# Optimization experiments

Measured on AMD Instinct MI355X. Metric: run time of the kernel, lower is better.

The kernel has to match this reference:

```python
import jax, jax.numpy as jnp
import numpy as np

B, N, C = 32, 197, 768   # batch, tokens (num_patches+1), emb_dim
KW = 197                 # kw_dim = seq_len
L = 12                   # num_layers (weights shared, norms per-layer)
HID = 3072               # mlp hidden = 4*emb_dim


def layer_norm(x, g, b, eps=1e-5):
    mu = jnp.mean(x, axis=-1, keepdims=True)
    var = jnp.var(x, axis=-1, keepdims=True)
    return (x - mu) * jax.lax.rsqrt(var + eps) * g + b


def attention(x, qkv_w, fc_w, fc_b, ln_g, ln_b, fc2_w, fc2_b, num_heads):
    b, n, c = x.shape
    d = c // num_heads
    qkv = (x @ qkv_w).reshape(b, n, 3, num_heads, d)
    q = qkv[:, :, 0].transpose(0, 2, 1, 3)  # [B,H,N,d]
    k = qkv[:, :, 1].transpose(0, 2, 1, 3)
    v = qkv[:, :, 2].transpose(0, 2, 1, 3)
    scale = d ** -0.5
    attn = jnp.einsum('bhnd,bhmd->bhnm', q, k) * scale      # [B,H,N,N]
    attn = attn @ fc_w + fc_b                                # [B,H,N,KW]
    attn = layer_norm(attn, ln_g, ln_b)
    attn = jax.nn.softmax(attn, axis=-1)
    attn = attn.transpose(0, 1, 3, 2)                        # [B,H,KW,N]
    y = jnp.einsum('bhkn,bhnd->bhkd', attn, v)               # [B,H,KW,d]
    # fc2 applied along KW axis of y.transpose(-2,-1): out[b,h,n,d]
    out = jnp.einsum('bhkd,kn->bnhd', y, fc2_w) + fc2_b[None, :, None, None]
    return out.reshape(b, n, c)


def mlp(x, w1, b1, w2, b2):
    return jax.nn.gelu(x @ w1 + b1, approximate=False) @ w2 + b2


def setup_inputs() -> dict:
    key = jax.random.key(0)
    ks = jax.random.split(key, 16)
    s = 0.02
    return {
        'x': jax.random.normal(ks[0], (B, N, C), jnp.float32),
        'qkv_w': jax.random.normal(ks[1], (C, 3 * C), jnp.float32) * s,
        'fc_w': jax.random.normal(ks[2], (N, KW), jnp.float32) * s,
        'fc_b': jnp.zeros((KW,), jnp.float32),
        'attn_ln_g': jnp.ones((KW,), jnp.float32),
        'attn_ln_b': jnp.zeros((KW,), jnp.float32),
        'fc2_w': jax.random.normal(ks[3], (KW, N), jnp.float32) * s,
        'fc2_b': jnp.zeros((N,), jnp.float32),
        'mlp_w1': jax.random.normal(ks[4], (C, HID), jnp.float32) * s,
        'mlp_b1': jnp.zeros((HID,), jnp.float32),
        'mlp_w2': jax.random.normal(ks[5], (HID, C), jnp.float32) * s,
        'mlp_b2': jnp.zeros((C,), jnp.float32),
        'f_ln_g': jnp.ones((L, C), jnp.float32),
        'f_ln_b': jnp.zeros((L, C), jnp.float32),
        'g_ln_g': jnp.ones((L, C), jnp.float32),
        'g_ln_b': jnp.zeros((L, C), jnp.float32),
        'num_heads': 12,
    }


def reference(x, qkv_w, fc_w, fc_b, attn_ln_g, attn_ln_b, fc2_w, fc2_b,
              mlp_w1, mlp_b1, mlp_w2, mlp_b2, f_ln_g, f_ln_b, g_ln_g, g_ln_b,
              num_heads):
    # x -> cat([x,x]) -> reversible stack -> mean of the two halves
    x1, x2 = x, x
    n_layers = f_ln_g.shape[0]
    for i in range(n_layers):
        # y1 = x1 + f(x2); y2 = x2 + g(y1)  (PreNorm wraps f and g)
        y1 = x1 + attention(layer_norm(x2, f_ln_g[i], f_ln_b[i]),
                            qkv_w, fc_w, fc_b, attn_ln_g, attn_ln_b,
                            fc2_w, fc2_b, num_heads)
        y2 = x2 + mlp(layer_norm(y1, g_ln_g[i], g_ln_b[i]),
                      mlp_w1, mlp_b1, mlp_w2, mlp_b2)
        x1, x2 = y1, y2
    return (x1 + x2) * 0.5
```

## Files before the change

### kernel.cpp

```cpp
#include <hip/hip_runtime.h>
#include <math.h>

#define BB   32
#define NN   197
#define CC   768
#define HH   12
#define DD   64
#define KWW  197
#define HIDD 3072
#define NL   12
#define RR   (BB*NN)
#define BHH  (BB*HH)
#define NP   224
#define SLS  232

typedef __attribute__((ext_vector_type(8))) short short8;
typedef __attribute__((ext_vector_type(4))) float floatx4;
typedef __attribute__((ext_vector_type(4))) unsigned short us4;

__device__ __forceinline__ unsigned short f2bf(float f) {
    unsigned int u = __float_as_uint(f);
    u += 0x7fff + ((u >> 16) & 1);
    return (unsigned short)(u >> 16);
}

__global__ void ln768_kernel(const float* __restrict__ in, const float* __restrict__ g,
                             const float* __restrict__ be, unsigned short* __restrict__ out) {
    int row = blockIdx.x;
    int t = threadIdx.x;
    float4 v = ((const float4*)(in + (size_t)row * CC))[t];
    float s = v.x+v.y+v.z+v.w;
    float q = v.x*v.x+v.y*v.y+v.z*v.z+v.w*v.w;
    for (int off = 1; off < 64; off <<= 1) {
        s += __shfl_xor(s, off, 64);
        q += __shfl_xor(q, off, 64);
    }
    __shared__ float sh[6];
    int wv = t >> 6, ln = t & 63;
    if (ln == 0) { sh[wv] = s; sh[3+wv] = q; }
    __syncthreads();
    s = sh[0]+sh[1]+sh[2];
    q = sh[3]+sh[4]+sh[5];
    float mu  = s * (1.0f/CC);
    float var = q * (1.0f/CC) - mu*mu;
    float rs  = rsqrtf(var + 1e-5f);
    float4 gv = ((const float4*)g)[t];
    float4 bv = ((const float4*)be)[t];
    us4 o = { f2bf((v.x-mu)*rs*gv.x + bv.x), f2bf((v.y-mu)*rs*gv.y + bv.y),
              f2bf((v.z-mu)*rs*gv.z + bv.z), f2bf((v.w-mu)*rs*gv.w + bv.w) };
    *(us4*)(out + (size_t)row*CC + t*4) = o;
}

__global__ void init_ln(const float* __restrict__ x, float* __restrict__ x1,
                        float* __restrict__ x2,
                        const float* __restrict__ g, const float* __restrict__ be,
                        unsigned short* __restrict__ out) {
    int row = blockIdx.x;
    int t = threadIdx.x;
    float4 v = ((const float4*)(x + (size_t)row * CC))[t];
    ((float4*)(x1 + (size_t)row * CC))[t] = v;
    ((float4*)(x2 + (size_t)row * CC))[t] = v;
    float s = v.x+v.y+v.z+v.w;
    float q = v.x*v.x+v.y*v.y+v.z*v.z+v.w*v.w;
    for (int off = 1; off < 64; off <<= 1) {
        s += __shfl_xor(s, off, 64);
        q += __shfl_xor(q, off, 64);
    }
    __shared__ float sh[6];
    int wv = t >> 6, ln = t & 63;
    if (ln == 0) { sh[wv] = s; sh[3+wv] = q; }
    __syncthreads();
    s = sh[0]+sh[1]+sh[2];
    q = sh[3]+sh[4]+sh[5];
    float mu  = s * (1.0f/CC);
    float var = q * (1.0f/CC) - mu*mu;
    float rs  = rsqrtf(var + 1e-5f);
    float4 gv = ((const float4*)g)[t];
    float4 bv = ((const float4*)be)[t];
    us4 o = { f2bf((v.x-mu)*rs*gv.x + bv.x), f2bf((v.y-mu)*rs*gv.y + bv.y),
              f2bf((v.z-mu)*rs*gv.z + bv.z), f2bf((v.w-mu)*rs*gv.w + bv.w) };
    *(us4*)(out + (size_t)row*CC + t*4) = o;
}

__global__ void reduce_ln(float* __restrict__ x2, const float* __restrict__ part,
                          const float* __restrict__ b2,
                          const float* __restrict__ g, const float* __restrict__ be,
                          unsigned short* __restrict__ out,
                          const float* __restrict__ x1f, float* __restrict__ outf,
                          int mode) {
    int row = blockIdx.x;
    int t = threadIdx.x;
    float4 v  = ((float4*)(x2 + (size_t)row * CC))[t];
    float4 a0 = ((const float4*)(part + (size_t)row * CC))[t];
    float4 a1 = ((const float4*)(part + (size_t)RR*CC + (size_t)row * CC))[t];
    float4 bb = ((const float4*)b2)[t];
    v.x += a0.x + a1.x + bb.x;
    v.y += a0.y + a1.y + bb.y;
    v.z += a0.z + a1.z + bb.z;
    v.w += a0.w + a1.w + bb.w;
    ((float4*)(x2 + (size_t)row * CC))[t] = v;
    if (mode == 2) {
        float4 xo = ((const float4*)(x1f + (size_t)row * CC))[t];
        float4 o;
        o.x = 0.5f*(xo.x + v.x); o.y = 0.5f*(xo.y + v.y);
        o.z = 0.5f*(xo.z + v.z); o.w = 0.5f*(xo.w + v.w);
        ((float4*)(outf + (size_t)row * CC))[t] = o;
        return;
    }
    float s = v.x+v.y+v.z+v.w;
    float q = v.x*v.x+v.y*v.y+v.z*v.z+v.w*v.w;
    for (int off = 1; off < 64; off <<= 1) {
        s += __shfl_xor(s, off, 64);
        q += __shfl_xor(q, off, 64);
    }
    __shared__ float sh[6];
    int wv = t >> 6, ln = t & 63;
    if (ln == 0) { sh[wv] = s; sh[3+wv] = q; }
    __syncthreads();
    s = sh[0]+sh[1]+sh[2];
    q = sh[3]+sh[4]+sh[5];
    float mu  = s * (1.0f/CC);
    float var = q * (1.0f/CC) - mu*mu;
    float rs  = rsqrtf(var + 1e-5f);
    float4 gv = ((const float4*)g)[t];
    float4 bv = ((const float4*)be)[t];
    us4 o = { f2bf((v.x-mu)*rs*gv.x + bv.x), f2bf((v.y-mu)*rs*gv.y + bv.y),
              f2bf((v.z-mu)*rs*gv.z + bv.z), f2bf((v.w-mu)*rs*gv.w + bv.w) };
    *(us4*)(out + (size_t)row*CC + t*4) = o;
}

__global__ void transpose_cast(const float* __restrict__ in, unsigned short* __restrict__ out,
                               int K, int Nd, int Kpad) {
    __shared__ float tile[32][33];
    int n0 = blockIdx.x*32, k0 = blockIdx.y*32;
    int tx = threadIdx.x & 31, ty = threadIdx.x >> 5;
    #pragma unroll
    for (int i = 0; i < 4; i++) {
        int k = k0 + ty + i*8;
        tile[ty + i*8][tx] = (k < K && n0+tx < Nd) ? in[(size_t)k*Nd + n0 + tx] : 0.f;
    }
    __syncthreads();
    #pragma unroll
    for (int i = 0; i < 4; i++) {
        int n = n0 + ty + i*8;
        if (n < Nd && k0 + tx < Kpad) out[(size_t)n*Kpad + k0 + tx] = f2bf(tile[tx][ty + i*8]);
    }
}

template<int EPI, int KS>
__global__ __launch_bounds__(256) void gemm128(
    const unsigned short* __restrict__ A, const unsigned short* __restrict__ Bt,
    const float* __restrict__ bias, float* __restrict__ Cf, unsigned short* __restrict__ Cb,
    int M, int Nd, int K)
{
    __shared__ unsigned short As[128*64];
    __shared__ unsigned short Bs[128*64];
    int tid  = threadIdx.x;
    int wv   = tid >> 6, lane = tid & 63;
    int wm   = wv >> 1, wn = wv & 1;
    int quad = lane >> 4, mrow = lane & 15;
    int rl   = lane >> 3, ps = lane & 7;

    int gx   = gridDim.x;
    int nwg  = gx * gridDim.y;
    int orig = blockIdx.y * gx + blockIdx.x;
    int qq = nwg >> 3, rr = nwg & 7;
    int xcd = orig & 7, idx = orig >> 3;
    int wg  = (xcd < rr ? xcd*(qq+1) : rr*(qq+1) + (xcd-rr)*qq) + idx;
    int bm  = (wg / gx) * 128;
    int bn  = (wg % gx) * 128;

    const int Kc    = K / KS;
    const int kbase = (KS > 1) ? blockIdx.z * Kc : 0;

    floatx4 acc[4][4];
    #pragma unroll
    for (int i = 0; i < 4; i++)
        #pragma unroll
        for (int j = 0; j < 4; j++) acc[i][j] = (floatx4){0.f,0.f,0.f,0.f};

    for (int k0 = kbase; k0 < kbase + Kc; k0 += 64) {
        #pragma unroll
        for (int i = 0; i < 4; i++) {
            int r_ = wv*32 + i*8 + rl;
            int sl = ps ^ (r_ & 7);
            int gr = bm + r_; if (gr > M-1) gr = M-1;
            __builtin_amdgcn_global_load_lds(
                (const __attribute__((address_space(1))) void*)(A + (size_t)gr*K + k0 + sl*8),
                (__attribute__((address_space(3))) void*)(As + (wv*32 + i*8)*64),
                16, 0, 0);
        }
        #pragma unroll
        for (int i = 0; i < 4; i++) {
            int r_ = wv*32 + i*8 + rl;
            int sl = ps ^ (r_ & 7);
            int gr = bn + r_;
            __builtin_amdgcn_global_load_lds(
                (const __attribute__((address_space(1))) void*)(Bt + (size_t)gr*K + k0 + sl*8),
                (__attribute__((address_space(3))) void*)(Bs + (wv*32 + i*8)*64),
                16, 0, 0);
        }
        __syncthreads();
        #pragma unroll
        for (int kk = 0; kk < 2; kk++) {
            short8 af[4], bf[4];
            #pragma unroll
            for (int mi = 0; mi < 4; mi++) {
                int lr = wm*64 + mi*16 + mrow;
                af[mi] = *(const short8*)&As[lr*64 + (((kk<<2)|quad) ^ (lr & 7))*8];
            }
            #pragma unroll
            for (int ni = 0; ni < 4; ni++) {
                int lr = wn*64 + ni*16 + mrow;
                bf[ni] = *(const short8*)&Bs[lr*64 + (((kk<<2)|quad) ^ (lr & 7))*8];
            }
            #pragma unroll
            for (int mi = 0; mi < 4; mi++)
                #pragma unroll
                for (int ni = 0; ni < 4; ni++)
                    acc[mi][ni] = __builtin_amdgcn_mfma_f32_16x16x32_bf16(
                        af[mi], bf[ni], acc[mi][ni], 0, 0, 0);
        }
        __syncthreads();
    }

    float* Cfz = (EPI == 5) ? (Cf + (size_t)blockIdx.z * M * Nd) : Cf;
    #pragma unroll
    for (int mi = 0; mi < 4; mi++) {
        int row0 = bm + wm*64 + mi*16 + quad*4;
        int bA[4], nA[4];
        if (EPI == 4) {
            int b0 = row0 / NN, n0 = row0 - b0*NN;
            #pragma unroll
            for (int r = 0; r < 4; r++) {
                bA[r] = b0; nA[r] = n0;
                n0++; if (n0 == NN) { n0 = 0; b0++; }
            }
        }
        #pragma unroll
        for (int ni = 0; ni < 4; ni++) {
            int col = bn + wn*64 + ni*16 + mrow;
            float bv = (EPI == 2) ? bias[col] : 0.f;
            #pragma unroll
            for (int r = 0; r < 4; r++) {
                int row = row0 + r;
                if (row >= M) continue;
                float v = acc[mi][ni][r] + bv;
                if (EPI == 2) {
                    v = v / (1.0f + __expf(-1.5957691216f*v*(1.0f + 0.044715f*v*v)));
                    Cb[(size_t)row*Nd + col] = f2bf(v);
                } else if (EPI == 5) {
                    Cfz[(size_t)row*Nd + col] = v;
                } else if (EPI == 4) {
                    int sel = col / CC;
                    int rem = col - sel*CC;
                    int h = rem >> 6, d = rem & 63;
                    int bh = bA[r]*HH + h;
                    unsigned short val = f2bf(v);
                    if (sel < 2)
                        Cb[((size_t)sel*BHH + bh)*NN*DD + (size_t)nA[r]*DD + d] = val;
                    else
                        Cb[(size_t)2*BHH*NN*DD + (size_t)bh*DD*NP + (size_t)d*NP + nA[r]] = val;
                }
            }
        }
    }
}

__global__ __launch_bounds__(256) void attn_score(
    const unsigned short* __restrict__ qb,
    const unsigned short* __restrict__ kb,
    const unsigned short* __restrict__ fw,
    const float* __restrict__ fbias,
    const float* __restrict__ g, const float* __restrict__ be,
    unsigned short* __restrict__ PT)
{
    int bh = blockIdx.y;
    int bm = blockIdx.x * 64;
    __shared__ unsigned short Ks[224*DD];
    __shared__ unsigned short S1s[64*SLS];
    __shared__ unsigned short Bs[224*32];
    __shared__ float gls[NP], bls[NP], bbs[NP];
    int tid = threadIdx.x;
    if (tid < NP) {
        bool vc = tid < KWW;
        gls[tid] = vc ? g[tid]     : 1.f;
        bls[tid] = vc ? be[tid]    : 0.f;
        bbs[tid] = vc ? fbias[tid] : 0.f;
    }
    int wv = tid >> 6, lane = tid & 63;
    int quad = lane >> 4, mrow = lane & 15;

    {
        int lrow = lane >> 3, lsl = lane & 7;
        #pragma unroll
        for (int i = 0; i < 7; i++) {
            int r = wv*56 + i*8 + lrow;
            int lko = (lsl ^ (r & 7)) * 8;
            __builtin_amdgcn_global_load_lds(
                (const __attribute__((address_space(1))) void*)(kb + ((size_t)bh*NN + r)*DD + lko),
                (__attribute__((address_space(3))) void*)(Ks + (size_t)(wv*56 + i*8)*DD),
                16, 0, 0);
        }
    }
    int qrow = bm + wv*16 + mrow; if (qrow > NN-1) qrow = NN-1;
    short8 aq0 = *(const short8*)&qb[((size_t)bh*NN + qrow)*DD + quad*8];
    short8 aq1 = *(const short8*)&qb[((size_t)bh*NN + qrow)*DD + 32 + quad*8];
    __syncthreads();

    #pragma unroll
    for (int ni = 0; ni < 14; ni++) {
        floatx4 a = (floatx4){0.f,0.f,0.f,0.f};
        int lr = ni*16 + mrow;
        short8 bf0 = *(const short8*)&Ks[(size_t)lr*DD + ((quad    ) ^ (lr & 7))*8];
        short8 bf1 = *(const short8*)&Ks[(size_t)lr*DD + ((4 + quad) ^ (lr & 7))*8];
        a = __builtin_amdgcn_mfma_f32_16x16x32_bf16(aq0, bf0, a, 0, 0, 0);
        a = __builtin_amdgcn_mfma_f32_16x16x32_bf16(aq1, bf1, a, 0, 0, 0);
        #pragma unroll
        for (int r = 0; r < 4; r++)
            S1s[(size_t)(wv*16 + quad*4 + r)*SLS + ni*16 + mrow] = f2bf(a[r]*0.125f);
    }
    __syncthreads();

    floatx4 acc[14];
    #pragma unroll
    for (int j = 0; j < 14; j++) acc[j] = (floatx4){0.f,0.f,0.f,0.f};
    for (int k0 = 0; k0 < 7; k0++) {
        for (int c = wv; c < 14; c += 4) {
            int r_ = c*16 + (lane >> 2);
            int gr = r_; if (gr > KWW-1) gr = KWW-1;
            int sl = ((lane & 3) ^ (r_ & 3)) * 8;
            __builtin_amdgcn_global_load_lds(
                (const __attribute__((address_space(1))) void*)(fw + (size_t)gr*NP + k0*32 + sl),
                (__attribute__((address_space(3))) void*)(Bs + (size_t)(c*16)*32),
                16, 0, 0);
        }
        __syncthreads();
        short8 af = *(const short8*)&S1s[(size_t)(wv*16 + mrow)*SLS + k0*32 + quad*8];
        #pragma unroll
        for (int ni = 0; ni < 14; ni++) {
            int lr = ni*16 + mrow;
            short8 bf = *(const short8*)&Bs[(size_t)lr*32 + (quad ^ (lr & 3))*8];
            acc[ni] = __builtin_amdgcn_mfma_f32_16x16x32_bf16(af, bf, acc[ni], 0, 0, 0);
        }
        __syncthreads();
    }

    float s[4] = {}, q[4] = {};
    #pragma unroll
    for (int ni = 0; ni < 14; ni++) {
        int col = ni*16 + mrow;
        float cm = (col < KWW) ? 1.f : 0.f;
        #pragma unroll
        for (int r = 0; r < 4; r++) {
            float x = acc[ni][r] + bbs[col];
            acc[ni][r] = x;
            s[r] += x*cm; q[r] += x*x*cm;
        }
    }
    #pragma unroll
    for (int o = 1; o < 16; o <<= 1)
        #pragma unroll
        for (int r = 0; r < 4; r++) {
            s[r] += __shfl_xor(s[r], o, 64);
            q[r] += __shfl_xor(q[r], o, 64);
        }
    float mu[4], rs[4], mx[4];
    #pragma unroll
    for (int r = 0; r < 4; r++) {
        mu[r] = s[r] * (1.0f/KWW);
        float var = q[r] * (1.0f/KWW) - mu[r]*mu[r];
        rs[r] = rsqrtf(var + 1e-5f);
        mx[r] = -1e30f;
    }
    #pragma unroll
    for (int ni = 0; ni < 14; ni++) {
        int col = ni*16 + mrow;
        bool vc = col < KWW;
        #pragma unroll
        for (int r = 0; r < 4; r++) {
            float x = (acc[ni][r] - mu[r]) * rs[r] * gls[col] + bls[col];
            acc[ni][r] = x;
            if (vc) mx[r] = fmaxf(mx[r], x);
        }
    }
    #pragma unroll
    for (int o = 1; o < 16; o <<= 1)
        #pragma unroll
        for (int r = 0; r < 4; r++)
            mx[r] = fmaxf(mx[r], __shfl_xor(mx[r], o, 64));
    float se[4] = {};
    #pragma unroll
    for (int ni = 0; ni < 14; ni++) {
        int col = ni*16 + mrow;
        float cm = (col < KWW) ? 1.f : 0.f;
        #pragma unroll
        for (int r = 0; r < 4; r++) {
            float p = __expf(acc[ni][r] - mx[r]) * cm;
            acc[ni][r] = p;
            se[r] += p;
        }
    }
    #pragma unroll
    for (int o = 1; o < 16; o <<= 1)
        #pragma unroll
        for (int r = 0; r < 4; r++)
            se[r] += __shfl_xor(se[r], o, 64);
    unsigned short* Pb = PT + (size_t)bh*NP*NP;
    int row0 = bm + wv*16 + quad*4;
    float inv0 = 1.0f/se[0], inv1 = 1.0f/se[1], inv2 = 1.0f/se[2], inv3 = 1.0f/se[3];
    #pragma unroll
    for (int ni = 0; ni < 14; ni++) {
        int col = ni*16 + mrow;
        if (col >= KWW) continue;
        if (row0 + 3 < NN) {
            us4 o = { f2bf(acc[ni][0]*inv0), f2bf(acc[ni][1]*inv1),
                      f2bf(acc[ni][2]*inv2), f2bf(acc[ni][3]*inv3) };
            *(us4*)&Pb[(size_t)col*NP + row0] = o;
        } else {
            float invs[4] = {inv0, inv1, inv2, inv3};
            #pragma unroll
            for (int r = 0; r < 4; r++)
                if (row0 + r < NN)
                    Pb[(size_t)col*NP + row0 + r] = f2bf(acc[ni][r]*invs[r]);
        }
    }
}

__global__ __launch_bounds__(256) void attn_out2(
    const unsigned short* __restrict__ PT,
    const unsigned short* __restrict__ vT,
    const unsigned short* __restrict__ fw,
    const float* __restrict__ bias,
    float* __restrict__ x1)
{
    int dt = blockIdx.x;
    int bh = blockIdx.y; int b = bh / HH, h = bh - b*HH;
    __shared__ unsigned short yT[16*232];
    int wv = threadIdx.x >> 6, lane = threadIdx.x & 63;
    int quad = lane >> 4, mrow = lane & 15;
    const unsigned short* Pb = PT + (size_t)bh*NP*NP;
    const unsigned short* Vb = vT + (size_t)bh*DD*NP + (size_t)(dt*16)*NP;

    short8 bfv[7];
    #pragma unroll
    for (int kc = 0; kc < 7; kc++)
        bfv[kc] = *(const short8*)&Vb[(size_t)mrow*NP + kc*32 + quad*8];
    #pragma unroll
    for (int i = 0; i < 2; i++) {
        int t0 = wv + i*8, t1 = t0 + 4;
        bool v1 = t1 < 14;
        floatx4 a0 = (floatx4){0.f,0.f,0.f,0.f};
        floatx4 a1 = (floatx4){0.f,0.f,0.f,0.f};
        #pragma unroll
        for (int kc = 0; kc < 7; kc++) {
            short8 p0 = *(const short8*)&Pb[(size_t)(t0*16 + mrow)*NP + kc*32 + quad*8];
            a0 = __builtin_amdgcn_mfma_f32_16x16x32_bf16(p0, bfv[kc], a0, 0, 0, 0);
            if (v1) {
                short8 p1 = *(const short8*)&Pb[(size_t)(t1*16 + mrow)*NP + kc*32 + quad*8];
                a1 = __builtin_amdgcn_mfma_f32_16x16x32_bf16(p1, bfv[kc], a1, 0, 0, 0);
            }
        }
        us4 o0 = { f2bf(a0[0]), f2bf(a0[1]), f2bf(a0[2]), f2bf(a0[3]) };
        *(us4*)&yT[mrow*232 + t0*16 + quad*4] = o0;
        if (v1) {
            us4 o1 = { f2bf(a1[0]), f2bf(a1[1]), f2bf(a1[2]), f2bf(a1[3]) };
            *(us4*)&yT[mrow*232 + t1*16 + quad*4] = o1;
        }
    }
    __syncthreads();

    short8 yf[7];
    #pragma unroll
    for (int kc = 0; kc < 7; kc++)
        yf[kc] = *(const short8*)&yT[mrow*232 + kc*32 + quad*8];
    float* xb = x1 + (size_t)b*NN*CC + (size_t)h*DD + dt*16 + mrow;
    #pragma unroll
    for (int i = 0; i < 2; i++) {
        int n0t = wv + i*8, n1t = n0t + 4;
        bool v1 = n1t < 13;
        floatx4 a0 = (floatx4){0.f,0.f,0.f,0.f};
        floatx4 a1 = (floatx4){0.f,0.f,0.f,0.f};
        #pragma unroll
        for (int kc = 0; kc < 7; kc++) {
            short8 f0 = *(const short8*)&fw[(size_t)(n0t*16 + mrow)*NP + kc*32 + quad*8];
            a0 = __builtin_amdgcn_mfma_f32_16x16x32_bf16(f0, yf[kc], a0, 0, 0, 0);
            if (v1) {
                short8 f1 = *(const short8*)&fw[(size_t)(n1t*16 + mrow)*NP + kc*32 + quad*8];
                a1 = __builtin_amdgcn_mfma_f32_16x16x32_bf16(f1, yf[kc], a1, 0, 0, 0);
            }
        }
        #pragma unroll
        for (int r = 0; r < 4; r++) {
            int n = n0t*16 + quad*4 + r;
            if (n < NN) xb[(size_t)n*CC] += a0[r] + bias[n];
        }
        if (v1) {
            #pragma unroll
            for (int r = 0; r < 4; r++) {
                int n = n1t*16 + quad*4 + r;
                if (n < NN) xb[(size_t)n*CC] += a1[r] + bias[n];
            }
        }
    }
}

extern "C" void kernel_launch(void* const* d_in, const int* in_sizes, int n_in,
                              void* d_out, int out_size, void* d_ws, size_t ws_size,
                              hipStream_t stream) {
    const float* x     = (const float*)d_in[0];
    const float* qkv_w = (const float*)d_in[1];
    const float* fc_w  = (const float*)d_in[2];
    const float* fc_b  = (const float*)d_in[3];
    const float* alng  = (const float*)d_in[4];
    const float* alnb  = (const float*)d_in[5];
    const float* fc2w  = (const float*)d_in[6];
    const float* fc2b  = (const float*)d_in[7];
    const float* w1    = (const float*)d_in[8];
    const float* b1    = (const float*)d_in[9];
    const float* w2    = (const float*)d_in[10];
    const float* b2    = (const float*)d_in[11];
    const float* flng  = (const float*)d_in[12];
    const float* flnb  = (const float*)d_in[13];
    const float* glng  = (const float*)d_in[14];
    const float* glnb  = (const float*)d_in[15];
    float* out = (float*)d_out;

    float* ws = (float*)d_ws;
    size_t off = 0;
    float* x1 = ws + off; off += (size_t)RR*CC;
    float* x2 = ws + off; off += (size_t)RR*CC;
    float* part = ws + off; off += (size_t)2*RR*CC;
    unsigned short* lnb = (unsigned short*)(ws + off); off += (size_t)RR*CC/2;
    unsigned short* qkvo = (unsigned short*)(ws + off);
    unsigned short* qb = qkvo;
    unsigned short* kb = qkvo + (size_t)BHH*NN*DD;
    unsigned short* vT = qkvo + (size_t)2*BHH*NN*DD;
    off += ((size_t)2*BHH*NN*DD + (size_t)BHH*DD*NP + 1) / 2;
    unsigned short* PT   = (unsigned short*)(ws + off); off += (size_t)BHH*NP*NP/2;
    unsigned short* hid  = (unsigned short*)(ws + off); off += (size_t)RR*HIDD/2;
    unsigned short* qkv_wt = (unsigned short*)(ws + off); off += (size_t)3*CC*CC/2;
    unsigned short* w1t    = (unsigned short*)(ws + off); off += (size_t)CC*HIDD/2;
    unsigned short* w2t    = (unsigned short*)(ws + off); off += (size_t)CC*HIDD/2;
    unsigned short* fc_wt  = (unsigned short*)(ws + off); off += (size_t)NP*NP/2 + 16;
    unsigned short* fc2_wt = (unsigned short*)(ws + off); off += (size_t)NP*NP/2 + 16;

    hipMemsetAsync(vT, 0, (size_t)BHH*DD*NP*2, stream);
    hipMemsetAsync(fc_wt, 0, (size_t)NP*NP*2, stream);
    hipMemsetAsync(fc2_wt, 0, (size_t)NP*NP*2, stream);

    transpose_cast<<<dim3(72, 24), 256, 0, stream>>>(qkv_w, qkv_wt, CC, 3*CC, CC);
    transpose_cast<<<dim3(96, 24), 256, 0, stream>>>(w1, w1t, CC, HIDD, CC);
    transpose_cast<<<dim3(24, 96), 256, 0, stream>>>(w2, w2t, HIDD, CC, HIDD);
    transpose_cast<<<dim3(7, 7),   256, 0, stream>>>(fc_w,  fc_wt,  NN, KWW, NP);
    transpose_cast<<<dim3(7, 7),   256, 0, stream>>>(fc2w,  fc2_wt, KWW, NN, NP);

    init_ln<<<RR, 192, 0, stream>>>(x, x1, x2, flng, flnb, lnb);

    const int MT = (RR + 127) / 128;
    for (int l = 0; l < NL; l++) {
        gemm128<4,1><<<dim3(3*CC/128, MT), 256, 0, stream>>>(
            lnb, qkv_wt, nullptr, nullptr, qb, RR, 3*CC, CC);
        attn_score<<<dim3(4, BHH), 256, 0, stream>>>(
            qb, kb, fc_wt, fc_b, alng, alnb, PT);
        attn_out2<<<dim3(4, BHH), 256, 0, stream>>>(PT, vT, fc2_wt, fc2b, x1);
        ln768_kernel<<<RR, 192, 0, stream>>>(x1, glng + l*CC, glnb + l*CC, lnb);
        gemm128<2,1><<<dim3(HIDD/128, MT), 256, 0, stream>>>(
            lnb, w1t, b1, nullptr, hid, RR, HIDD, CC);
        gemm128<5,2><<<dim3(CC/128, MT, 2), 256, 0, stream>>>(
            hid, w2t, nullptr, part, nullptr, RR, CC, HIDD);
        if (l + 1 < NL) {
            reduce_ln<<<RR, 192, 0, stream>>>(
                x2, part, b2, flng + (l+1)*CC, flnb + (l+1)*CC, lnb,
                nullptr, nullptr, 1);
        } else {
            reduce_ln<<<RR, 192, 0, stream>>>(
                x2, part, b2, nullptr, nullptr, nullptr, x1, out, 2);
        }
    }
}
```

Before: 3.336 ms.

## Double-buffer GEMM K-tiles and widen attention output blocks to two d-tiles

The GEMM main loop now uses two 32-wide K stages in LDS, ping-ponging between buffers. The next tile's global-to-LDS load is issued before computing the current tile, so memory latency overlaps with MFMA work. Separately, each attn_out2 block now handles two 16-wide d tiles. This reuses each loaded P and fc2 fragment for two MFMAs and halves the grid. The risks are more barriers per K step with half-size tiles, fewer blocks for attn_out2, and higher register use.

```diff
diff --git a/kernel.cpp b/kernel.cpp
--- a/kernel.cpp
+++ b/kernel.cpp
@@ -153,13 +153,13 @@
     const float* __restrict__ bias, float* __restrict__ Cf, unsigned short* __restrict__ Cb,
     int M, int Nd, int K)
 {
-    __shared__ unsigned short As[128*64];
-    __shared__ unsigned short Bs[128*64];
+    __shared__ unsigned short As0[128*32], As1[128*32];
+    __shared__ unsigned short Bs0[128*32], Bs1[128*32];
     int tid  = threadIdx.x;
     int wv   = tid >> 6, lane = tid & 63;
     int wm   = wv >> 1, wn = wv & 1;
     int quad = lane >> 4, mrow = lane & 15;
-    int rl   = lane >> 3, ps = lane & 7;
+    int rl   = lane >> 2, ps = lane & 3;
 
     int gx   = gridDim.x;
     int nwg  = gx * gridDim.y;
@@ -172,6 +172,7 @@
 
     const int Kc    = K / KS;
     const int kbase = (KS > 1) ? blockIdx.z * Kc : 0;
+    const int nt    = Kc / 32;
 
     floatx4 acc[4][4];
     #pragma unroll
@@ -179,50 +180,63 @@
         #pragma unroll
         for (int j = 0; j < 4; j++) acc[i][j] = (floatx4){0.f,0.f,0.f,0.f};
 
-    for (int k0 = kbase; k0 < kbase + Kc; k0 += 64) {
-        #pragma unroll
-        for (int i = 0; i < 4; i++) {
-            int r_ = wv*32 + i*8 + rl;
-            int sl = ps ^ (r_ & 7);
-            int gr = bm + r_; if (gr > M-1) gr = M-1;
-            __builtin_amdgcn_global_load_lds(
-                (const __attribute__((address_space(1))) void*)(A + (size_t)gr*K + k0 + sl*8),
-                (__attribute__((address_space(3))) void*)(As + (wv*32 + i*8)*64),
-                16, 0, 0);
-        }
-        #pragma unroll
-        for (int i = 0; i < 4; i++) {
-            int r_ = wv*32 + i*8 + rl;
-            int sl = ps ^ (r_ & 7);
-            int gr = bn + r_;
-            __builtin_amdgcn_global_load_lds(
-                (const __attribute__((address_space(1))) void*)(Bt + (size_t)gr*K + k0 + sl*8),
-                (__attribute__((address_space(3))) void*)(Bs + (wv*32 + i*8)*64),
-                16, 0, 0);
-        }
+#define G_STAGE(Aa, Bb, kcol)                                                     \
+    do {                                                                          \
+        _Pragma("unroll")                                                         \
+        for (int i_ = 0; i_ < 2; i_++) {                                          \
+            int r_ = wv*32 + i_*16 + rl;                                          \
+            int sl_ = ps ^ ((r_ >> 2) & 3);                                       \
+            int gr_ = bm + r_; if (gr_ > M-1) gr_ = M-1;                          \
+            __builtin_amdgcn_global_load_lds(                                     \
+                (const __attribute__((address_space(1))) void*)(A + (size_t)gr_*K + (kcol) + sl_*8), \
+                (__attribute__((address_space(3))) void*)(Aa + (wv*32 + i_*16)*32), \
+                16, 0, 0);                                                        \
+        }                                                                         \
+        _Pragma("unroll")                                                         \
+        for (int i_ = 0; i_ < 2; i_++) {                                          \
+            int r_ = wv*32 + i_*16 + rl;                                          \
+            int sl_ = ps ^ ((r_ >> 2) & 3);                                       \
+            int gr_ = bn + r_;                                                    \
+            __builtin_amdgcn_global_load_lds(                                     \
+                (const __attribute__((address_space(1))) void*)(Bt + (size_t)gr_*K + (kcol) + sl_*8), \
+                (__attribute__((address_space(3))) void*)(Bb + (wv*32 + i_*16)*32), \
+                16, 0, 0);                                                        \
+        }                                                                         \
+    } while (0)
+
+#define G_COMP(Aa, Bb)                                                            \
+    do {                                                                          \
+        short8 af[4], bf[4];                                                      \
+        _Pragma("unroll")                                                         \
+        for (int mi = 0; mi < 4; mi++) {                                          \
+            int lr = wm*64 + mi*16 + mrow;                                        \
+            af[mi] = *(const short8*)&Aa[lr*32 + (quad ^ ((lr >> 2) & 3))*8];     \
+        }                                                                         \
+        _Pragma("unroll")                                                         \
+        for (int ni = 0; ni < 4; ni++) {                                          \
+            int lr = wn*64 + ni*16 + mrow;                                        \
+            bf[ni] = *(const short8*)&Bb[lr*32 + (quad ^ ((lr >> 2) & 3))*8];     \
+        }                                                                         \
+        _Pragma("unroll")                                                         \
+        for (int mi = 0; mi < 4; mi++)                                            \
+            _Pragma("unroll")                                                     \
+            for (int ni = 0; ni < 4; ni++)                                        \
+                acc[mi][ni] = __builtin_amdgcn_mfma_f32_16x16x32_bf16(            \
+                    af[mi], bf[ni], acc[mi][ni], 0, 0, 0);                        \
+    } while (0)
+
+    G_STAGE(As0, Bs0, kbase);
+    __syncthreads();
+    for (int t = 0; t < nt; t += 2) {
+        if (t + 1 < nt) G_STAGE(As1, Bs1, kbase + (t+1)*32);
+        G_COMP(As0, Bs0);
         __syncthreads();
-        #pragma unroll
-        for (int kk = 0; kk < 2; kk++) {
-            short8 af[4], bf[4];
-            #pragma unroll
-            for (int mi = 0; mi < 4; mi++) {
-                int lr = wm*64 + mi*16 + mrow;
-                af[mi] = *(const short8*)&As[lr*64 + (((kk<<2)|quad) ^ (lr & 7))*8];
-            }
-            #pragma unroll
-            for (int ni = 0; ni < 4; ni++) {
-                int lr = wn*64 + ni*16 + mrow;
-                bf[ni] = *(const short8*)&Bs[lr*64 + (((kk<<2)|quad) ^ (lr & 7))*8];
-            }
-            #pragma unroll
-            for (int mi = 0; mi < 4; mi++)
-                #pragma unroll
-                for (int ni = 0; ni < 4; ni++)
-                    acc[mi][ni] = __builtin_amdgcn_mfma_f32_16x16x32_bf16(
-                        af[mi], bf[ni], acc[mi][ni], 0, 0, 0);
-        }
+        if (t + 2 < nt) G_STAGE(As0, Bs0, kbase + (t+2)*32);
+        if (t + 1 < nt) G_COMP(As1, Bs1);
         __syncthreads();
     }
+#undef G_STAGE
+#undef G_COMP
 
     float* Cfz = (EPI == 5) ? (Cf + (size_t)blockIdx.z * M * Nd) : Cf;
     #pragma unroll
@@ -434,72 +448,66 @@
     const float* __restrict__ bias,
     float* __restrict__ x1)
 {
-    int dt = blockIdx.x;
+    int dt0 = blockIdx.x * 2;
     int bh = blockIdx.y; int b = bh / HH, h = bh - b*HH;
-    __shared__ unsigned short yT[16*232];
+    __shared__ unsigned short yT[32*232];
     int wv = threadIdx.x >> 6, lane = threadIdx.x & 63;
     int quad = lane >> 4, mrow = lane & 15;
     const unsigned short* Pb = PT + (size_t)bh*NP*NP;
-    const unsigned short* Vb = vT + (size_t)bh*DD*NP + (size_t)(dt*16)*NP;
-
-    short8 bfv[7];
-    #pragma unroll
-    for (int kc = 0; kc < 7; kc++)
-        bfv[kc] = *(const short8*)&Vb[(size_t)mrow*NP + kc*32 + quad*8];
-    #pragma unroll
-    for (int i = 0; i < 2; i++) {
-        int t0 = wv + i*8, t1 = t0 + 4;
-        bool v1 = t1 < 14;
-        floatx4 a0 = (floatx4){0.f,0.f,0.f,0.f};
-        floatx4 a1 = (floatx4){0.f,0.f,0.f,0.f};
-        #pragma unroll
-        for (int kc = 0; kc < 7; kc++) {
-            short8 p0 = *(const short8*)&Pb[(size_t)(t0*16 + mrow)*NP + kc*32 + quad*8];
-            a0 = __builtin_amdgcn_mfma_f32_16x16x32_bf16(p0, bfv[kc], a0, 0, 0, 0);
-            if (v1) {
-                short8 p1 = *(const short8*)&Pb[(size_t)(t1*16 + mrow)*NP + kc*32 + quad*8];
-                a1 = __builtin_amdgcn_mfma_f32_16x16x32_bf16(p1, bfv[kc], a1, 0, 0, 0);
+    const unsigned short* Vb = vT + (size_t)bh*DD*NP + (size_t)(dt0*16)*NP;
+
+    short8 bv0[7], bv1[7];
+    #pragma unroll
+    for (int kc = 0; kc < 7; kc++) {
+        bv0[kc] = *(const short8*)&Vb[(size_t)mrow*NP + kc*32 + quad*8];
+        bv1[kc] = *(const short8*)&Vb[(size_t)(16 + mrow)*NP + kc*32 + quad*8];
+    }
+    #pragma unroll
+    for (int i = 0; i < 4; i++) {
+        int t0 = wv + i*4;
+        if (t0 < 14) {
+            floatx4 a0 = (floatx4){0.f,0.f,0.f,0.f};
+            floatx4 a1 = (floatx4){0.f,0.f,0.f,0.f};
+            #pragma unroll
+            for (int kc = 0; kc < 7; kc++) {
+                short8 p0 = *(const short8*)&Pb[(size_t)(t0*16 + mrow)*NP + kc*32 + quad*8];
+                a0 = __builtin_amdgcn_mfma_f32_16x16x32_bf16(p0, bv0[kc], a0, 0, 0, 0);
+                a1 = __builtin_amdgcn_mfma_f32_16x16x32_bf16(p0, bv1[kc], a1, 0, 0, 0);
             }
-        }
-        us4 o0 = { f2bf(a0[0]), f2bf(a0[1]), f2bf(a0[2]), f2bf(a0[3]) };
-        *(us4*)&yT[mrow*232 + t0*16 + quad*4] = o0;
-        if (v1) {
+            us4 o0 = { f2bf(a0[0]), f2bf(a0[1]), f2bf(a0[2]), f2bf(a0[3]) };
             us4 o1 = { f2bf(a1[0]), f2bf(a1[1]), f2bf(a1[2]), f2bf(a1[3]) };
-            *(us4*)&yT[mrow*232 + t1*16 + quad*4] = o1;
-        }
-    }
-    __syncthreads();
-
-    short8 yf[7];
-    #pragma unroll
-    for (int kc = 0; kc < 7; kc++)
-        yf[kc] = *(const short8*)&yT[mrow*232 + kc*32 + quad*8];
-    float* xb = x1 + (size_t)b*NN*CC + (size_t)h*DD + dt*16 + mrow;
-    #pragma unroll
-    for (int i = 0; i < 2; i++) {
-        int n0t = wv + i*8, n1t = n0t + 4;
-        bool v1 = n1t < 13;
-        floatx4 a0 = (floatx4){0.f,0.f,0.f,0.f};
-        floatx4 a1 = (floatx4){0.f,0.f,0.f,0.f};
-        #pragma unroll
-        for (int kc = 0; kc < 7; kc++) {
-            short8 f0 = *(const short8*)&fw[(size_t)(n0t*16 + mrow)*NP + kc*32 + quad*8];
-            a0 = __builtin_amdgcn_mfma_f32_16x16x32_bf16(f0, yf[kc], a0, 0, 0, 0);
-            if (v1) {
-                short8 f1 = *(const short8*)&fw[(size_t)(n1t*16 + mrow)*NP + kc*32 + quad*8];
-                a1 = __builtin_amdgcn_mfma_f32_16x16x32_bf16(f1, yf[kc], a1, 0, 0, 0);
+            *(us4*)&yT[(size_t)mrow*232 + t0*16 + quad*4] = o0;
+            *(us4*)&yT[(size_t)(16 + mrow)*232 + t0*16 + quad*4] = o1;
+        }
+    }
+    __syncthreads();
+
+    short8 yf0[7], yf1[7];
+    #pragma unroll
+    for (int kc = 0; kc < 7; kc++) {
+        yf0[kc] = *(const short8*)&yT[(size_t)mrow*232 + kc*32 + quad*8];
+        yf1[kc] = *(const short8*)&yT[(size_t)(16 + mrow)*232 + kc*32 + quad*8];
+    }
+    float* xb = x1 + (size_t)b*NN*CC + (size_t)h*DD + dt0*16 + mrow;
+    #pragma unroll
+    for (int i = 0; i < 4; i++) {
+        int n0t = wv + i*4;
+        if (n0t < 13) {
+            floatx4 a0 = (floatx4){0.f,0.f,0.f,0.f};
+            floatx4 a1 = (floatx4){0.f,0.f,0.f,0.f};
+            #pragma unroll
+            for (int kc = 0; kc < 7; kc++) {
+                short8 f0 = *(const short8*)&fw[(size_t)(n0t*16 + mrow)*NP + kc*32 + quad*8];
+                a0 = __builtin_amdgcn_mfma_f32_16x16x32_bf16(f0, yf0[kc], a0, 0, 0, 0);
+                a1 = __builtin_amdgcn_mfma_f32_16x16x32_bf16(f0, yf1[kc], a1, 0, 0, 0);
             }
-        }
-        #pragma unroll
-        for (int r = 0; r < 4; r++) {
-            int n = n0t*16 + quad*4 + r;
-            if (n < NN) xb[(size_t)n*CC] += a0[r] + bias[n];
-        }
-        if (v1) {
             #pragma unroll
             for (int r = 0; r < 4; r++) {
-                int n = n1t*16 + quad*4 + r;
-                if (n < NN) xb[(size_t)n*CC] += a1[r] + bias[n];
+                int n = n0t*16 + quad*4 + r;
+                if (n < NN) {
+                    xb[(size_t)n*CC]      += a0[r] + bias[n];
+                    xb[(size_t)n*CC + 16] += a1[r] + bias[n];
+                }
             }
         }
     }
@@ -563,7 +571,7 @@
             lnb, qkv_wt, nullptr, nullptr, qb, RR, 3*CC, CC);
         attn_score<<<dim3(4, BHH), 256, 0, stream>>>(
             qb, kb, fc_wt, fc_b, alng, alnb, PT);
-        attn_out2<<<dim3(4, BHH), 256, 0, stream>>>(PT, vT, fc2_wt, fc2b, x1);
+        attn_out2<<<dim3(2, BHH), 256, 0, stream>>>(PT, vT, fc2_wt, fc2b, x1);
         ln768_kernel<<<RR, 192, 0, stream>>>(x1, glng + l*CC, glnb + l*CC, lnb);
         gemm128<2,1><<<dim3(HIDD/128, MT), 256, 0, stream>>>(
             lnb, w1t, b1, nullptr, hid, RR, HIDD, CC);
```

Result: slower. 3.594 ms (+7.7%).
